# Optimization experiments

Measured on AMD Instinct MI355X. Metric: run time of the kernel, lower is better.

## Reference

```python
import jax, jax.numpy as jnp
import numpy as np

E, H, DK, DV = 768, 12, 64, 64
S, B = 8, 1024


def setup_inputs() -> dict:
    key = jax.random.key(0)
    ks = jax.random.split(key, 12)
    std = 1.0 / np.sqrt(E)
    inp = {
        "Q": jax.random.normal(ks[0], (S, B, E), jnp.float32),
        "K": jax.random.normal(ks[1], (S, B, E), jnp.float32),
        "V": jax.random.normal(ks[2], (S, B, E), jnp.float32),
        # projection weights, torch Linear convention: y = x @ W.T + b
        "Wq": jax.random.normal(ks[3], (H * DK, E), jnp.float32) * std,
        "bq": jax.random.normal(ks[4], (H * DK,), jnp.float32) * std,
        "Wk": jax.random.normal(ks[5], (H * DK, E), jnp.float32) * std,
        "bk": jax.random.normal(ks[6], (H * DK,), jnp.float32) * std,
        "Wv": jax.random.normal(ks[7], (H * DV, E), jnp.float32) * std,
        "bv": jax.random.normal(ks[8], (H * DV,), jnp.float32) * std,
        "Wo": jax.random.normal(ks[9], (E, H * DV), jnp.float32) * std,
        "bo": jax.random.normal(ks[10], (E,), jnp.float32) * std,
        "ln_g": jnp.ones((E,), jnp.float32),
        "ln_b": jnp.zeros((E,), jnp.float32),
    }
    return inp


def _attention(Q, K, V, Wq, bq, Wk, bk, Wv, bv, Wo, bo, ln_g, ln_b):
    s, b, _ = Q.shape
    # linear projections, then view(S,B,H,d).transpose(1,2) -> [S,H,B,d]
    q = (Q @ Wq.T + bq).reshape(s, b, H, DK).transpose(0, 2, 1, 3)
    k = (K @ Wk.T + bk).reshape(s, b, H, DK).transpose(0, 2, 1, 3)
    v = (V @ Wv.T + bv).reshape(s, b, H, DV).transpose(0, 2, 1, 3)
    # scores over the batch (size-B) axis: [S,H,B,B]
    scores = jnp.einsum("shbd,shcd->shbc", q, k) / jnp.sqrt(
        jnp.asarray(DK, jnp.float32))
    attn = jax.nn.softmax(scores, axis=-1)
    context = jnp.einsum("shbc,shcd->shbd", attn, v)  # [S,H,B,DV]
    context = context.transpose(0, 2, 1, 3).reshape(s, b, H * DV)
    out = context @ Wo.T + bo
    x = out + Q  # residual
    mu = jnp.mean(x, axis=-1, keepdims=True)
    var = jnp.mean((x - mu) ** 2, axis=-1, keepdims=True)
    normed = (x - mu) * jax.lax.rsqrt(var + 1e-5) * ln_g + ln_b
    return normed, attn


def reference(Q, K, V, Wq, bq, Wk, bk, Wv, bv, Wo, bo, ln_g, ln_b):
    return _attention(Q, K, V, Wq, bq, Wk, bk, Wv, bv, Wo, bo, ln_g, ln_b)
```

## Files before the change

kernel.cpp:

```cpp
#include <hip/hip_runtime.h>
#include <hip/hip_bf16.h>
#include <math.h>

#define Sd 8
#define Bd 1024
#define Ed 768
#define Hd 12
#define Dd 64
#define SBd 8192

typedef short bf16x8 __attribute__((ext_vector_type(8)));
typedef unsigned short u16x8 __attribute__((ext_vector_type(8)));
typedef float f32x4 __attribute__((ext_vector_type(4)));

#define QSC 0.18033688011112043f

#define BARRIER()                                        \
  do {                                                   \
    asm volatile("s_waitcnt lgkmcnt(0)" ::: "memory");   \
    __builtin_amdgcn_s_barrier();                        \
    asm volatile("" ::: "memory");                       \
  } while (0)

static __device__ __forceinline__ unsigned short f2bf(float f) {
  __hip_bfloat16 h = __float2bfloat16(f);
  unsigned short u;
  __builtin_memcpy(&u, &h, 2);
  return u;
}

static __device__ __forceinline__ unsigned int pk2(float lo, float hi) {
  __hip_bfloat162 h = __float22bfloat162_rn(make_float2(lo, hi));
  unsigned int u;
  __builtin_memcpy(&u, &h, 4);
  return u;
}

__global__ __launch_bounds__(256, 2) void qkv_kernel(
    const float* __restrict__ Qin, const float* __restrict__ Kin,
    const float* __restrict__ Vin,
    const float* __restrict__ Wq, const float* __restrict__ bq,
    const float* __restrict__ Wk, const float* __restrict__ bk,
    const float* __restrict__ Wv, const float* __restrict__ bv,
    unsigned short* __restrict__ qo, unsigned short* __restrict__ ko,
    unsigned short* __restrict__ vo) {
  __shared__ unsigned short As[128 * 72];
  __shared__ unsigned short Bs[128 * 72];
  const float* X;
  const float* W;
  const float* bias;
  switch (blockIdx.z) {
    case 0: X = Qin; W = Wq; bias = bq; break;
    case 1: X = Kin; W = Wk; bias = bk; break;
    default: X = Vin; W = Wv; bias = bv; break;
  }
  const int i0 = blockIdx.x * 128;
  const int j0 = blockIdx.y * 128;
  const int t = threadIdx.x;
  const int w = t >> 6, l = t & 63, lr = l & 15, lg = l >> 4;
  const int wr = w >> 1, wc = w & 1;

  f32x4 acc[4][4] = {};

  for (int k0 = 0; k0 < Ed; k0 += 64) {
    uint2 pa[8], pb[8];
#pragma unroll
    for (int q = 0; q < 8; ++q) {
      int flat = t + 256 * q;
      int row = flat >> 4;
      int c4 = (flat & 15) * 4;
      float4 va = *(const float4*)(X + (size_t)(i0 + row) * Ed + k0 + c4);
      float4 vb = *(const float4*)(W + (size_t)(j0 + row) * Ed + k0 + c4);
      pa[q] = make_uint2(pk2(va.x, va.y), pk2(va.z, va.w));
      pb[q] = make_uint2(pk2(vb.x, vb.y), pk2(vb.z, vb.w));
    }
    __syncthreads();
#pragma unroll
    for (int q = 0; q < 8; ++q) {
      int flat = t + 256 * q;
      int row = flat >> 4;
      int c4 = (flat & 15) * 4;
      *(uint2*)&As[row * 72 + c4] = pa[q];
      *(uint2*)&Bs[row * 72 + c4] = pb[q];
    }
    __syncthreads();
#pragma unroll
    for (int ks = 0; ks < 2; ++ks) {
      bf16x8 af[4], bf[4];
#pragma unroll
      for (int fr = 0; fr < 4; ++fr)
        af[fr] = *(const bf16x8*)&As[(wr * 64 + fr * 16 + lr) * 72 + ks * 32 + lg * 8];
#pragma unroll
      for (int fc = 0; fc < 4; ++fc)
        bf[fc] = *(const bf16x8*)&Bs[(wc * 64 + fc * 16 + lr) * 72 + ks * 32 + lg * 8];
#pragma unroll
      for (int fr = 0; fr < 4; ++fr)
#pragma unroll
        for (int fc = 0; fc < 4; ++fc)
          acc[fr][fc] = __builtin_amdgcn_mfma_f32_16x16x32_bf16(af[fr], bf[fc], acc[fr][fc], 0, 0, 0);
    }
  }

  const int z = blockIdx.z;
  if (z < 2) {
    unsigned short* out = (z == 0) ? qo : ko;
    const float sc = (z == 0) ? QSC : 1.0f;
#pragma unroll
    for (int fr = 0; fr < 4; ++fr) {
#pragma unroll
      for (int fc = 0; fc < 4; ++fc) {
        int colg = j0 + wc * 64 + fc * 16 + lr;
        int h = colg >> 6, d = colg & 63;
        float bv_ = bias[colg];
#pragma unroll
        for (int r = 0; r < 4; ++r) {
          int i = i0 + wr * 64 + fr * 16 + lg * 4 + r;
          int s = i >> 10, b = i & 1023;
          float v = (acc[fr][fc][r] + bv_) * sc;
          out[((((size_t)s * Hd + h) * Bd + b) << 6) + d] = f2bf(v);
        }
      }
    }
  } else {
#pragma unroll
    for (int fr = 0; fr < 4; ++fr) {
#pragma unroll
      for (int fc = 0; fc < 4; ++fc) {
        int colg = j0 + wc * 64 + fc * 16 + lr;
        int h = colg >> 6, d = colg & 63;
        float bv_ = bias[colg];
#pragma unroll
        for (int r = 0; r < 4; ++r) {
          int i = i0 + wr * 64 + fr * 16 + lg * 4 + r;
          int s = i >> 10, b = i & 1023;
          float v = acc[fr][fc][r] + bv_;
          vo[(((size_t)s * Hd + h) * 64 + d) * Bd + b] = f2bf(v);
        }
      }
    }
  }
}

__global__ __launch_bounds__(512) void attn_kernel(
    const unsigned short* __restrict__ qb, const unsigned short* __restrict__ kb,
    const unsigned short* __restrict__ vt, float* __restrict__ attn_out,
    unsigned short* __restrict__ ctx_out) {
  __shared__ unsigned short Ks[64 * 72];
  __shared__ unsigned short Vs[64 * 72];
  __shared__ unsigned short Pb[8][16 * 72];
  const int sh = blockIdx.x;
  const int s = sh / Hd, h = sh % Hd;
  const int row0 = blockIdx.y * 128;
  const size_t base = (size_t)sh * Bd * 64;
  const int t = threadIdx.x;
  const int w = t >> 6, l = t & 63, lr = l & 15, lg = l >> 4;
  const int srow = t >> 3, skg = (t & 7) * 8;

  const int qrow = row0 + w * 16 + lr;
  const bf16x8 aq0 = *(const bf16x8*)(qb + base + (size_t)qrow * 64 + lg * 8);
  const bf16x8 aq1 = *(const bf16x8*)(qb + base + (size_t)qrow * 64 + 32 + lg * 8);

  float lsum[4] = {0.f, 0.f, 0.f, 0.f};

  {
    const unsigned short* kp = kb + base + (size_t)srow * 64 + skg;
    u16x8 k0 = *(const u16x8*)kp;
    for (int ct = 0; ct < 16; ++ct) {
      BARRIER();
      *(u16x8*)&Ks[srow * 72 + skg] = k0;
      BARRIER();
      if (ct < 15) {
        const unsigned short* kn = kb + base + (size_t)((ct + 1) * 64 + srow) * 64 + skg;
        k0 = *(const u16x8*)kn;
      }
      f32x4 scv[4] = {};
#pragma unroll
      for (int ks = 0; ks < 2; ++ks) {
        bf16x8 a = ks ? aq1 : aq0;
#pragma unroll
        for (int c2 = 0; c2 < 4; ++c2) {
          bf16x8 bb = *(const bf16x8*)&Ks[(c2 * 16 + lr) * 72 + ks * 32 + lg * 8];
          scv[c2] = __builtin_amdgcn_mfma_f32_16x16x32_bf16(a, bb, scv[c2], 0, 0, 0);
        }
      }
#pragma unroll
      for (int c2 = 0; c2 < 4; ++c2)
#pragma unroll
        for (int r = 0; r < 4; ++r)
          lsum[r] += __builtin_amdgcn_exp2f(scv[c2][r]);
    }
  }
#pragma unroll
  for (int r = 0; r < 4; ++r) {
    float s1 = lsum[r];
    s1 += __shfl_xor(s1, 1, 16);
    s1 += __shfl_xor(s1, 2, 16);
    s1 += __shfl_xor(s1, 4, 16);
    s1 += __shfl_xor(s1, 8, 16);
    lsum[r] = 1.0f / s1;
  }

  f32x4 cacc[4] = {};
  const unsigned short* vbase = vt + (size_t)sh * 64 * Bd;
  u16x8 k0, v0;
  {
    const unsigned short* kp = kb + base + (size_t)srow * 64 + skg;
    k0 = *(const u16x8*)kp;
    const unsigned short* vp = vbase + (size_t)srow * Bd + skg;
    v0 = *(const u16x8*)vp;
  }
  for (int ct = 0; ct < 16; ++ct) {
    BARRIER();
    *(u16x8*)&Ks[srow * 72 + skg] = k0;
    *(u16x8*)&Vs[srow * 72 + skg] = v0;
    BARRIER();
    if (ct < 15) {
      const unsigned short* kn = kb + base + (size_t)((ct + 1) * 64 + srow) * 64 + skg;
      k0 = *(const u16x8*)kn;
      const unsigned short* vn = vbase + (size_t)srow * Bd + (ct + 1) * 64 + skg;
      v0 = *(const u16x8*)vn;
    }
    f32x4 scv[4] = {};
#pragma unroll
    for (int ks = 0; ks < 2; ++ks) {
      bf16x8 a = ks ? aq1 : aq0;
#pragma unroll
      for (int c2 = 0; c2 < 4; ++c2) {
        bf16x8 bb = *(const bf16x8*)&Ks[(c2 * 16 + lr) * 72 + ks * 32 + lg * 8];
        scv[c2] = __builtin_amdgcn_mfma_f32_16x16x32_bf16(a, bb, scv[c2], 0, 0, 0);
      }
    }
#pragma unroll
    for (int c2 = 0; c2 < 4; ++c2) {
#pragma unroll
      for (int r = 0; r < 4; ++r) {
        float p = __builtin_amdgcn_exp2f(scv[c2][r]) * lsum[r];
        int row = row0 + w * 16 + lg * 4 + r;
        __builtin_nontemporal_store(
            p, &attn_out[((size_t)sh * Bd + row) * Bd + ct * 64 + c2 * 16 + lr]);
        Pb[w][(lg * 4 + r) * 72 + c2 * 16 + lr] = f2bf(p);
      }
    }
#pragma unroll
    for (int ks2 = 0; ks2 < 2; ++ks2) {
      bf16x8 pa = *(const bf16x8*)&Pb[w][lr * 72 + ks2 * 32 + lg * 8];
#pragma unroll
      for (int dt = 0; dt < 4; ++dt) {
        bf16x8 bv = *(const bf16x8*)&Vs[(dt * 16 + lr) * 72 + ks2 * 32 + lg * 8];
        cacc[dt] = __builtin_amdgcn_mfma_f32_16x16x32_bf16(pa, bv, cacc[dt], 0, 0, 0);
      }
    }
  }

#pragma unroll
  for (int dt = 0; dt < 4; ++dt) {
#pragma unroll
    for (int r = 0; r < 4; ++r) {
      int row = row0 + w * 16 + lg * 4 + r;
      size_t i = (size_t)s * Bd + row;
      int j = h * 64 + dt * 16 + lr;
      ctx_out[i * Ed + j] = f2bf(cacc[dt][r]);
    }
  }
}

__global__ __launch_bounds__(256, 2) void proj_kernel(
    const unsigned short* __restrict__ ctx, const float* __restrict__ Wo,
    const float* __restrict__ bo, const float* __restrict__ Qin,
    float* __restrict__ xout) {
  __shared__ unsigned short As[128 * 72];
  __shared__ unsigned short Bs[128 * 72];
  const int i0 = blockIdx.x * 128;
  const int j0 = blockIdx.y * 128;
  const int t = threadIdx.x;
  const int w = t >> 6, l = t & 63, lr = l & 15, lg = l >> 4;
  const int wr = w >> 1, wc = w & 1;

  f32x4 acc[4][4] = {};

  for (int k0 = 0; k0 < Ed; k0 += 64) {
    u16x8 pa[4];
    uint2 pb[8];
#pragma unroll
    for (int q = 0; q < 4; ++q) {
      int flat = t + 256 * q;
      int row = flat >> 3;
      int c8 = (flat & 7) * 8;
      pa[q] = *(const u16x8*)(ctx + (size_t)(i0 + row) * Ed + k0 + c8);
    }
#pragma unroll
    for (int q = 0; q < 8; ++q) {
      int flat = t + 256 * q;
      int row = flat >> 4;
      int c4 = (flat & 15) * 4;
      float4 vb = *(const float4*)(Wo + (size_t)(j0 + row) * Ed + k0 + c4);
      pb[q] = make_uint2(pk2(vb.x, vb.y), pk2(vb.z, vb.w));
    }
    __syncthreads();
#pragma unroll
    for (int q = 0; q < 4; ++q) {
      int flat = t + 256 * q;
      int row = flat >> 3;
      int c8 = (flat & 7) * 8;
      *(u16x8*)&As[row * 72 + c8] = pa[q];
    }
#pragma unroll
    for (int q = 0; q < 8; ++q) {
      int flat = t + 256 * q;
      int row = flat >> 4;
      int c4 = (flat & 15) * 4;
      *(uint2*)&Bs[row * 72 + c4] = pb[q];
    }
    __syncthreads();
#pragma unroll
    for (int ks = 0; ks < 2; ++ks) {
      bf16x8 af[4], bf[4];
#pragma unroll
      for (int fr = 0; fr < 4; ++fr)
        af[fr] = *(const bf16x8*)&As[(wr * 64 + fr * 16 + lr) * 72 + ks * 32 + lg * 8];
#pragma unroll
      for (int fc = 0; fc < 4; ++fc)
        bf[fc] = *(const bf16x8*)&Bs[(wc * 64 + fc * 16 + lr) * 72 + ks * 32 + lg * 8];
#pragma unroll
      for (int fr = 0; fr < 4; ++fr)
#pragma unroll
        for (int fc = 0; fc < 4; ++fc)
          acc[fr][fc] = __builtin_amdgcn_mfma_f32_16x16x32_bf16(af[fr], bf[fc], acc[fr][fc], 0, 0, 0);
    }
  }

#pragma unroll
  for (int fr = 0; fr < 4; ++fr) {
#pragma unroll
    for (int fc = 0; fc < 4; ++fc) {
      int j = j0 + wc * 64 + fc * 16 + lr;
      float bv_ = bo[j];
#pragma unroll
      for (int r = 0; r < 4; ++r) {
        int i = i0 + wr * 64 + fr * 16 + lg * 4 + r;
        float v = acc[fr][fc][r] + bv_ + Qin[(size_t)i * Ed + j];
        xout[(size_t)i * Ed + j] = v;
      }
    }
  }
}

__global__ __launch_bounds__(256) void ln_kernel(
    const float* __restrict__ x, const float* __restrict__ g,
    const float* __restrict__ bb, float* __restrict__ out) {
  const int i = blockIdx.x;
  const int t = threadIdx.x;
  const float* xr = x + (size_t)i * Ed;
  float v0 = xr[t], v1 = xr[t + 256], v2 = xr[t + 512];
  float s1 = v0 + v1 + v2;
  float s2 = v0 * v0 + v1 * v1 + v2 * v2;
#pragma unroll
  for (int mk = 1; mk < 64; mk <<= 1) {
    s1 += __shfl_xor(s1, mk, 64);
    s2 += __shfl_xor(s2, mk, 64);
  }
  __shared__ float red[8];
  const int w = t >> 6, l = t & 63;
  if (l == 0) { red[w] = s1; red[w + 4] = s2; }
  __syncthreads();
  s1 = red[0] + red[1] + red[2] + red[3];
  s2 = red[4] + red[5] + red[6] + red[7];
  float mu = s1 * (1.0f / 768.0f);
  float var = s2 * (1.0f / 768.0f) - mu * mu;
  float rs = rsqrtf(var + 1e-5f);
  float* orow = out + (size_t)i * Ed;
  orow[t] = (v0 - mu) * rs * g[t] + bb[t];
  orow[t + 256] = (v1 - mu) * rs * g[t + 256] + bb[t + 256];
  orow[t + 512] = (v2 - mu) * rs * g[t + 512] + bb[t + 512];
}

extern "C" void kernel_launch(void* const* d_in, const int* in_sizes, int n_in,
                              void* d_out, int out_size, void* d_ws, size_t ws_size,
                              hipStream_t stream) {
  (void)in_sizes; (void)n_in; (void)out_size; (void)ws_size;
  const float* Qin = (const float*)d_in[0];
  const float* Kin = (const float*)d_in[1];
  const float* Vin = (const float*)d_in[2];
  const float* Wq = (const float*)d_in[3];
  const float* bq = (const float*)d_in[4];
  const float* Wk = (const float*)d_in[5];
  const float* bk = (const float*)d_in[6];
  const float* Wv = (const float*)d_in[7];
  const float* bv = (const float*)d_in[8];
  const float* Wo = (const float*)d_in[9];
  const float* bo = (const float*)d_in[10];
  const float* ln_g = (const float*)d_in[11];
  const float* ln_b = (const float*)d_in[12];

  float* outp = (float*)d_out;
  float* normed = outp;
  float* attn_out = outp + (size_t)SBd * Ed;

  char* ws = (char*)d_ws;
  unsigned short* qws = (unsigned short*)ws;
  unsigned short* kws = qws + 6291456;
  unsigned short* vws = kws + 6291456;
  unsigned short* ctxws = vws + 6291456;
  float* xws = (float*)(ws + (size_t)4 * 12582912);

  hipLaunchKernelGGL(qkv_kernel, dim3(64, 6, 3), dim3(256), 0, stream,
                     Qin, Kin, Vin, Wq, bq, Wk, bk, Wv, bv, qws, kws, vws);
  hipLaunchKernelGGL(attn_kernel, dim3(96, 8), dim3(512), 0, stream,
                     qws, kws, vws, attn_out, ctxws);
  hipLaunchKernelGGL(proj_kernel, dim3(64, 6), dim3(256), 0, stream,
                     ctxws, Wo, bo, Qin, xws);
  hipLaunchKernelGGL(ln_kernel, dim3(8192), dim3(256), 0, stream,
                     xws, ln_g, ln_b, normed);
}
```

Baseline: 266.3 us.

## Store K/V in MFMA fragment order and read directly from global

The QKV projection epilogue now writes K and V in a pre-swizzled layout that matches the MFMA B-operand fragment order. Each lane can then load its bf16x8 operand with one contiguous 16-byte global read. The attention kernel drops the shared-memory staging of K and V along with the barriers around it, reading fragments straight from global memory and L2. This removes LDS traffic and block-wide syncs, but each wave now issues its own global loads with no explicit prefetch, so load latency may be exposed. The V epilogue also packs four bf16 values per store.

After: 285.2 us. 7.1% more time.

```diff
diff --git a/kernel.cpp b/kernel.cpp
--- a/kernel.cpp
+++ b/kernel.cpp
@@ -14,13 +14,6 @@
 typedef float f32x4 __attribute__((ext_vector_type(4)));
 
 #define QSC 0.18033688011112043f
-
-#define BARRIER()                                        \
-  do {                                                   \
-    asm volatile("s_waitcnt lgkmcnt(0)" ::: "memory");   \
-    __builtin_amdgcn_s_barrier();                        \
-    asm volatile("" ::: "memory");                       \
-  } while (0)
 
 static __device__ __forceinline__ unsigned short f2bf(float f) {
   __hip_bfloat16 h = __float2bfloat16(f);
@@ -102,9 +95,7 @@
   }
 
   const int z = blockIdx.z;
-  if (z < 2) {
-    unsigned short* out = (z == 0) ? qo : ko;
-    const float sc = (z == 0) ? QSC : 1.0f;
+  if (z == 0) {
 #pragma unroll
     for (int fr = 0; fr < 4; ++fr) {
 #pragma unroll
@@ -116,37 +107,60 @@
         for (int r = 0; r < 4; ++r) {
           int i = i0 + wr * 64 + fr * 16 + lg * 4 + r;
           int s = i >> 10, b = i & 1023;
-          float v = (acc[fr][fc][r] + bv_) * sc;
-          out[((((size_t)s * Hd + h) * Bd + b) << 6) + d] = f2bf(v);
+          float v = (acc[fr][fc][r] + bv_) * QSC;
+          qo[((((size_t)s * Hd + h) * Bd + b) << 6) + d] = f2bf(v);
         }
       }
     }
-  } else {
-#pragma unroll
-    for (int fr = 0; fr < 4; ++fr) {
-#pragma unroll
-      for (int fc = 0; fc < 4; ++fc) {
-        int colg = j0 + wc * 64 + fc * 16 + lr;
-        int h = colg >> 6, d = colg & 63;
-        float bv_ = bias[colg];
+  } else if (z == 1) {
+    const int ctb = (i0 >> 6) + wr;
+#pragma unroll
+    for (int fc = 0; fc < 4; ++fc) {
+      int h = (j0 >> 6) + wc;
+      int d = fc * 16 + lr;
+      int ks = fc >> 1;
+      int lgd = (fc * 2 + (lr >> 3)) & 3;
+      int d8 = lr & 7;
+      float bv_ = bias[h * 64 + d];
+#pragma unroll
+      for (int fr = 0; fr < 4; ++fr) {
 #pragma unroll
         for (int r = 0; r < 4; ++r) {
           int i = i0 + wr * 64 + fr * 16 + lg * 4 + r;
-          int s = i >> 10, b = i & 1023;
-          float v = acc[fr][fc][r] + bv_;
-          vo[(((size_t)s * Hd + h) * 64 + d) * Bd + b] = f2bf(v);
+          int s = i >> 10;
+          int ct = ctb & 15;
+          int kvrow = fr * 16 + lg * 4 + r;
+          size_t off = (((((size_t)(s * Hd + h) * 16 + ct) * 2 + ks) * 4 + lgd) * 64 + kvrow) * 8 + d8;
+          ko[off] = f2bf(acc[fr][fc][r] + bv_);
         }
       }
     }
+  } else {
+    const int hv = (j0 >> 6) + wc;
+    const int s = (i0 + wr * 64) >> 10;
+    const int ct = ((i0 >> 6) + wr) & 15;
+    const int b8 = (lg & 1) * 4;
+#pragma unroll
+    for (int fr = 0; fr < 4; ++fr) {
+      int ks2 = fr >> 1;
+      int lg2 = (fr * 2 + (lg >> 1)) & 3;
+#pragma unroll
+      for (int fc = 0; fc < 4; ++fc) {
+        int dfeat = fc * 16 + lr;
+        float bv_ = bias[hv * 64 + dfeat];
+        uint2 pv = make_uint2(pk2(acc[fr][fc][0] + bv_, acc[fr][fc][1] + bv_),
+                              pk2(acc[fr][fc][2] + bv_, acc[fr][fc][3] + bv_));
+        size_t off = ((((size_t)(s * Hd + hv) * 16 + ct) * 2 + ks2) * 4 + lg2) * 64 + dfeat;
+        *(uint2*)&vo[off * 8 + b8] = pv;
+      }
+    }
   }
 }
 
 __global__ __launch_bounds__(512) void attn_kernel(
-    const unsigned short* __restrict__ qb, const unsigned short* __restrict__ kb,
-    const unsigned short* __restrict__ vt, float* __restrict__ attn_out,
+    const unsigned short* __restrict__ qb, const unsigned short* __restrict__ kf,
+    const unsigned short* __restrict__ vf, float* __restrict__ attn_out,
     unsigned short* __restrict__ ctx_out) {
-  __shared__ unsigned short Ks[64 * 72];
-  __shared__ unsigned short Vs[64 * 72];
   __shared__ unsigned short Pb[8][16 * 72];
   const int sh = blockIdx.x;
   const int s = sh / Hd, h = sh % Hd;
@@ -154,41 +168,32 @@
   const size_t base = (size_t)sh * Bd * 64;
   const int t = threadIdx.x;
   const int w = t >> 6, l = t & 63, lr = l & 15, lg = l >> 4;
-  const int srow = t >> 3, skg = (t & 7) * 8;
 
   const int qrow = row0 + w * 16 + lr;
   const bf16x8 aq0 = *(const bf16x8*)(qb + base + (size_t)qrow * 64 + lg * 8);
   const bf16x8 aq1 = *(const bf16x8*)(qb + base + (size_t)qrow * 64 + 32 + lg * 8);
 
+  const unsigned short* kbase = kf + base;
+  const unsigned short* vbase = vf + base;
+
   float lsum[4] = {0.f, 0.f, 0.f, 0.f};
 
-  {
-    const unsigned short* kp = kb + base + (size_t)srow * 64 + skg;
-    u16x8 k0 = *(const u16x8*)kp;
-    for (int ct = 0; ct < 16; ++ct) {
-      BARRIER();
-      *(u16x8*)&Ks[srow * 72 + skg] = k0;
-      BARRIER();
-      if (ct < 15) {
-        const unsigned short* kn = kb + base + (size_t)((ct + 1) * 64 + srow) * 64 + skg;
-        k0 = *(const u16x8*)kn;
-      }
-      f32x4 scv[4] = {};
-#pragma unroll
-      for (int ks = 0; ks < 2; ++ks) {
-        bf16x8 a = ks ? aq1 : aq0;
-#pragma unroll
-        for (int c2 = 0; c2 < 4; ++c2) {
-          bf16x8 bb = *(const bf16x8*)&Ks[(c2 * 16 + lr) * 72 + ks * 32 + lg * 8];
-          scv[c2] = __builtin_amdgcn_mfma_f32_16x16x32_bf16(a, bb, scv[c2], 0, 0, 0);
-        }
-      }
-#pragma unroll
-      for (int c2 = 0; c2 < 4; ++c2)
-#pragma unroll
-        for (int r = 0; r < 4; ++r)
-          lsum[r] += __builtin_amdgcn_exp2f(scv[c2][r]);
-    }
+  for (int ct = 0; ct < 16; ++ct) {
+    f32x4 scv[4] = {};
+#pragma unroll
+    for (int ks = 0; ks < 2; ++ks) {
+      bf16x8 a = ks ? aq1 : aq0;
+#pragma unroll
+      for (int c2 = 0; c2 < 4; ++c2) {
+        bf16x8 bb = *(const bf16x8*)(kbase + ((ct * 2 + ks) * 4 + lg) * 512 + (c2 * 16 + lr) * 8);
+        scv[c2] = __builtin_amdgcn_mfma_f32_16x16x32_bf16(a, bb, scv[c2], 0, 0, 0);
+      }
+    }
+#pragma unroll
+    for (int c2 = 0; c2 < 4; ++c2)
+#pragma unroll
+      for (int r = 0; r < 4; ++r)
+        lsum[r] += __builtin_amdgcn_exp2f(scv[c2][r]);
   }
 #pragma unroll
   for (int r = 0; r < 4; ++r) {
@@ -201,32 +206,14 @@
   }
 
   f32x4 cacc[4] = {};
-  const unsigned short* vbase = vt + (size_t)sh * 64 * Bd;
-  u16x8 k0, v0;
-  {
-    const unsigned short* kp = kb + base + (size_t)srow * 64 + skg;
-    k0 = *(const u16x8*)kp;
-    const unsigned short* vp = vbase + (size_t)srow * Bd + skg;
-    v0 = *(const u16x8*)vp;
-  }
   for (int ct = 0; ct < 16; ++ct) {
-    BARRIER();
-    *(u16x8*)&Ks[srow * 72 + skg] = k0;
-    *(u16x8*)&Vs[srow * 72 + skg] = v0;
-    BARRIER();
-    if (ct < 15) {
-      const unsigned short* kn = kb + base + (size_t)((ct + 1) * 64 + srow) * 64 + skg;
-      k0 = *(const u16x8*)kn;
-      const unsigned short* vn = vbase + (size_t)srow * Bd + (ct + 1) * 64 + skg;
-      v0 = *(const u16x8*)vn;
-    }
     f32x4 scv[4] = {};
 #pragma unroll
     for (int ks = 0; ks < 2; ++ks) {
       bf16x8 a = ks ? aq1 : aq0;
 #pragma unroll
       for (int c2 = 0; c2 < 4; ++c2) {
-        bf16x8 bb = *(const bf16x8*)&Ks[(c2 * 16 + lr) * 72 + ks * 32 + lg * 8];
+        bf16x8 bb = *(const bf16x8*)(kbase + ((ct * 2 + ks) * 4 + lg) * 512 + (c2 * 16 + lr) * 8);
         scv[c2] = __builtin_amdgcn_mfma_f32_16x16x32_bf16(a, bb, scv[c2], 0, 0, 0);
       }
     }
@@ -246,7 +233,7 @@
       bf16x8 pa = *(const bf16x8*)&Pb[w][lr * 72 + ks2 * 32 + lg * 8];
 #pragma unroll
       for (int dt = 0; dt < 4; ++dt) {
-        bf16x8 bv = *(const bf16x8*)&Vs[(dt * 16 + lr) * 72 + ks2 * 32 + lg * 8];
+        bf16x8 bv = *(const bf16x8*)(vbase + ((ct * 2 + ks2) * 4 + lg) * 512 + (dt * 16 + lr) * 8);
         cacc[dt] = __builtin_amdgcn_mfma_f32_16x16x32_bf16(pa, bv, cacc[dt], 0, 0, 0);
       }
     }
```

## Transpose score MFMA, double-buffer K/V LDS, shuffle P into registers instead of LDS

Applied to the files above, without the earlier changes.

Swaps the MFMA operand order so each lane holds four consecutive key columns of one query row. This allows the softmax sum to use two cross-group shuffles and lets the attention probabilities be written as 16-byte vector nontemporal stores. The K/V shared tiles are double-buffered, which removes one barrier per iteration. The per-wave P staging buffer in LDS is replaced by bf16 packing and lane shuffles that build the A operand for the PV MFMA. The cost is more shuffle instructions, and correctness depends on the new lane mapping.

New measurement: 273.6 us. 1.03x slower.

```diff
diff --git a/kernel.cpp b/kernel.cpp
--- a/kernel.cpp
+++ b/kernel.cpp
@@ -145,9 +145,8 @@
     const unsigned short* __restrict__ qb, const unsigned short* __restrict__ kb,
     const unsigned short* __restrict__ vt, float* __restrict__ attn_out,
     unsigned short* __restrict__ ctx_out) {
-  __shared__ unsigned short Ks[64 * 72];
-  __shared__ unsigned short Vs[64 * 72];
-  __shared__ unsigned short Pb[8][16 * 72];
+  __shared__ unsigned short Ks[2][64 * 72];
+  __shared__ unsigned short Vs[2][64 * 72];
   const int sh = blockIdx.x;
   const int s = sh / Hd, h = sh % Hd;
   const int row0 = blockIdx.y * 128;
@@ -160,65 +159,49 @@
   const bf16x8 aq0 = *(const bf16x8*)(qb + base + (size_t)qrow * 64 + lg * 8);
   const bf16x8 aq1 = *(const bf16x8*)(qb + base + (size_t)qrow * 64 + 32 + lg * 8);
 
-  float lsum[4] = {0.f, 0.f, 0.f, 0.f};
+  float lsum = 0.0f;
 
   {
-    const unsigned short* kp = kb + base + (size_t)srow * 64 + skg;
-    u16x8 k0 = *(const u16x8*)kp;
+    u16x8 kr = *(const u16x8*)(kb + base + (size_t)srow * 64 + skg);
     for (int ct = 0; ct < 16; ++ct) {
+      *(u16x8*)&Ks[ct & 1][srow * 72 + skg] = kr;
       BARRIER();
-      *(u16x8*)&Ks[srow * 72 + skg] = k0;
-      BARRIER();
-      if (ct < 15) {
-        const unsigned short* kn = kb + base + (size_t)((ct + 1) * 64 + srow) * 64 + skg;
-        k0 = *(const u16x8*)kn;
-      }
+      if (ct < 15)
+        kr = *(const u16x8*)(kb + base + (size_t)((ct + 1) * 64 + srow) * 64 + skg);
       f32x4 scv[4] = {};
 #pragma unroll
       for (int ks = 0; ks < 2; ++ks) {
         bf16x8 a = ks ? aq1 : aq0;
 #pragma unroll
         for (int c2 = 0; c2 < 4; ++c2) {
-          bf16x8 bb = *(const bf16x8*)&Ks[(c2 * 16 + lr) * 72 + ks * 32 + lg * 8];
-          scv[c2] = __builtin_amdgcn_mfma_f32_16x16x32_bf16(a, bb, scv[c2], 0, 0, 0);
+          bf16x8 kf = *(const bf16x8*)&Ks[ct & 1][(c2 * 16 + lr) * 72 + ks * 32 + lg * 8];
+          scv[c2] = __builtin_amdgcn_mfma_f32_16x16x32_bf16(kf, a, scv[c2], 0, 0, 0);
         }
       }
 #pragma unroll
       for (int c2 = 0; c2 < 4; ++c2)
 #pragma unroll
         for (int r = 0; r < 4; ++r)
-          lsum[r] += __builtin_amdgcn_exp2f(scv[c2][r]);
-    }
-  }
-#pragma unroll
-  for (int r = 0; r < 4; ++r) {
-    float s1 = lsum[r];
-    s1 += __shfl_xor(s1, 1, 16);
-    s1 += __shfl_xor(s1, 2, 16);
-    s1 += __shfl_xor(s1, 4, 16);
-    s1 += __shfl_xor(s1, 8, 16);
-    lsum[r] = 1.0f / s1;
-  }
+          lsum += __builtin_amdgcn_exp2f(scv[c2][r]);
+    }
+  }
+  lsum += __shfl_xor(lsum, 16, 64);
+  lsum += __shfl_xor(lsum, 32, 64);
+  const float invl = 1.0f / lsum;
 
   f32x4 cacc[4] = {};
   const unsigned short* vbase = vt + (size_t)sh * 64 * Bd;
-  u16x8 k0, v0;
-  {
-    const unsigned short* kp = kb + base + (size_t)srow * 64 + skg;
-    k0 = *(const u16x8*)kp;
-    const unsigned short* vp = vbase + (size_t)srow * Bd + skg;
-    v0 = *(const u16x8*)vp;
-  }
+  u16x8 kr, vr;
+  kr = *(const u16x8*)(kb + base + (size_t)srow * 64 + skg);
+  vr = *(const u16x8*)(vbase + (size_t)srow * Bd + skg);
+  float* arow = attn_out + ((size_t)sh * Bd + qrow) * Bd + lg * 4;
   for (int ct = 0; ct < 16; ++ct) {
-    BARRIER();
-    *(u16x8*)&Ks[srow * 72 + skg] = k0;
-    *(u16x8*)&Vs[srow * 72 + skg] = v0;
+    *(u16x8*)&Ks[ct & 1][srow * 72 + skg] = kr;
+    *(u16x8*)&Vs[ct & 1][srow * 72 + skg] = vr;
     BARRIER();
     if (ct < 15) {
-      const unsigned short* kn = kb + base + (size_t)((ct + 1) * 64 + srow) * 64 + skg;
-      k0 = *(const u16x8*)kn;
-      const unsigned short* vn = vbase + (size_t)srow * Bd + (ct + 1) * 64 + skg;
-      v0 = *(const u16x8*)vn;
+      kr = *(const u16x8*)(kb + base + (size_t)((ct + 1) * 64 + srow) * 64 + skg);
+      vr = *(const u16x8*)(vbase + (size_t)srow * Bd + (ct + 1) * 64 + skg);
     }
     f32x4 scv[4] = {};
 #pragma unroll
@@ -226,27 +209,42 @@
       bf16x8 a = ks ? aq1 : aq0;
 #pragma unroll
       for (int c2 = 0; c2 < 4; ++c2) {
-        bf16x8 bb = *(const bf16x8*)&Ks[(c2 * 16 + lr) * 72 + ks * 32 + lg * 8];
-        scv[c2] = __builtin_amdgcn_mfma_f32_16x16x32_bf16(a, bb, scv[c2], 0, 0, 0);
-      }
-    }
+        bf16x8 kf = *(const bf16x8*)&Ks[ct & 1][(c2 * 16 + lr) * 72 + ks * 32 + lg * 8];
+        scv[c2] = __builtin_amdgcn_mfma_f32_16x16x32_bf16(kf, a, scv[c2], 0, 0, 0);
+      }
+    }
+    float p[4][4];
+    unsigned int Upk[4][2];
 #pragma unroll
     for (int c2 = 0; c2 < 4; ++c2) {
 #pragma unroll
-      for (int r = 0; r < 4; ++r) {
-        float p = __builtin_amdgcn_exp2f(scv[c2][r]) * lsum[r];
-        int row = row0 + w * 16 + lg * 4 + r;
-        __builtin_nontemporal_store(
-            p, &attn_out[((size_t)sh * Bd + row) * Bd + ct * 64 + c2 * 16 + lr]);
-        Pb[w][(lg * 4 + r) * 72 + c2 * 16 + lr] = f2bf(p);
-      }
-    }
+      for (int r = 0; r < 4; ++r)
+        p[c2][r] = __builtin_amdgcn_exp2f(scv[c2][r]) * invl;
+      f32x4 stv = {p[c2][0], p[c2][1], p[c2][2], p[c2][3]};
+      __builtin_nontemporal_store(stv, (f32x4*)(arow + ct * 64 + c2 * 16));
+      Upk[c2][0] = pk2(p[c2][0], p[c2][1]);
+      Upk[c2][1] = pk2(p[c2][2], p[c2][3]);
+    }
+    const int lghalf = lg >> 1;
+    const int srcb = lr + 16 * ((lg & 1) * 2);
 #pragma unroll
     for (int ks2 = 0; ks2 < 2; ++ks2) {
-      bf16x8 pa = *(const bf16x8*)&Pb[w][lr * 72 + ks2 * 32 + lg * 8];
+      unsigned int pw[4];
+#pragma unroll
+      for (int t2 = 0; t2 < 2; ++t2) {
+#pragma unroll
+        for (int rp = 0; rp < 2; ++rp) {
+          int src = srcb + 16 * t2;
+          unsigned int sA = (unsigned int)__shfl((int)Upk[2 * ks2][rp], src, 64);
+          unsigned int sB = (unsigned int)__shfl((int)Upk[2 * ks2 + 1][rp], src, 64);
+          pw[t2 * 2 + rp] = lghalf ? sB : sA;
+        }
+      }
+      bf16x8 pa;
+      __builtin_memcpy(&pa, pw, 16);
 #pragma unroll
       for (int dt = 0; dt < 4; ++dt) {
-        bf16x8 bv = *(const bf16x8*)&Vs[(dt * 16 + lr) * 72 + ks2 * 32 + lg * 8];
+        bf16x8 bv = *(const bf16x8*)&Vs[ct & 1][(dt * 16 + lr) * 72 + ks2 * 32 + lg * 8];
         cacc[dt] = __builtin_amdgcn_mfma_f32_16x16x32_bf16(pa, bv, cacc[dt], 0, 0, 0);
       }
     }
```
